# Performance work log

Hardware: AMD Instinct MI355X
Metric: run time of the kernel (lower is better)

## Reference

```python
import jax, jax.numpy as jnp
import numpy as np

MX_D, MN_D, CENTERS, WIDTH, SLOPE = 10.0, 0.0, 16, 1.0, 0.01
T_STEPS = 3


def _lrelu(x):
    return jax.nn.leaky_relu(x, SLOPE)


def _gauss(d):
    # d: [B,E,1] distances -> [B,E,CENTERS] gaussian radial basis
    mu = jnp.linspace(MN_D, MX_D, CENTERS, dtype=d.dtype)
    return jnp.exp(-jnp.square((d - mu[None, None, :]) / WIDTH))


def _equiv_message(v, idx2, n_recv, W1, W2, b, aw, ab):
    # v: [B,E,F] = concat(sender feats, receiver feats, bond feats).
    # Outer-product expand over receiver-cell axis (einsum with one-hot),
    # permutation-equivariant linear (local term + cell-sum term), LeakyReLU,
    # gather receiver cell, sigmoid attention gate, scatter_add to receivers.
    B, E, _ = v.shape
    O = W1.shape[1]
    oh = jax.nn.one_hot(idx2, n_recv, dtype=v.dtype)                 # [E,N]
    y_loc = jnp.einsum('bef,fo->beo', v, W1)                          # per-cell term
    y_sum = jnp.einsum('bef,fo->beo', v, W2) + b                      # cell-sum term (sum_n v*oh = v)
    y = _lrelu(y_loc[..., None] * oh[None, :, None, :] + y_sum[..., None])  # [B,E,O,N]
    gidx = jnp.broadcast_to(idx2[None, :, None, None], (B, E, O, 1))
    lat = jnp.take_along_axis(y, gidx, axis=3)[..., 0]                # [B,E,O]
    lat = jax.nn.sigmoid(lat @ aw + ab[None, None, :]) * lat          # attention gating
    return jnp.zeros((B, n_recv, O), v.dtype).at[:, idx2].add(lat)    # scatter_add over receivers


def _forward(sites, bonds, sites_p, bonds_sp, bonds_ps,
             se_W, se_b, sep_W, sep_b, ee_W, ee_b, eep_W, eep_b,
             eq_W1_ss, eq_W2_ss, eq_b_ss, att_w_ss, att_b_ss,
             eq_W1_ps, eq_W2_ps, eq_b_ps, att_w_ps, att_b_ps,
             eq_W1_sp, eq_W2_sp, eq_b_sp, att_w_sp, att_b_sp,
             nu_W1, nu_b1, nu_W2, nu_b2, nup_W1, nup_b1, nup_W2, nup_b2,
             p1_W, p1_b, p2a_W, p2a_b, p2b_W, p2b_b, p3_W, p3_b,
             idx1, idx2, idx1_sp, idx2_sp, idx1_ps, idx2_ps):
    s = _lrelu(sites @ se_W + se_b)          # [B,N,D] site embedding
    sp = _lrelu(sites_p @ sep_W + sep_b)     # [B,Np,D] pore embedding
    be = _lrelu(_gauss(bonds) @ ee_W + ee_b)
    bsp = _lrelu(_gauss(bonds_sp) @ eep_W + eep_b)
    bps = _lrelu(_gauss(bonds_ps) @ eep_W + eep_b)
    N, Np = s.shape[1], sp.shape[1]
    for t in range(T_STEPS):  # fixed number of message-passing layers
        v_ss = jnp.concatenate([s[:, idx1], s[:, idx2], be], -1)
        m = _equiv_message(v_ss, idx2, N, eq_W1_ss[t], eq_W2_ss[t], eq_b_ss[t], att_w_ss[t], att_b_ss[t])
        v_ps = jnp.concatenate([sp[:, idx1_ps], s[:, idx2_ps], bps], -1)
        m_ps = _equiv_message(v_ps, idx2_ps, N, eq_W1_ps[t], eq_W2_ps[t], eq_b_ps[t], att_w_ps[t], att_b_ps[t])
        v_sp = jnp.concatenate([s[:, idx1_sp], sp[:, idx2_sp], bsp], -1)
        m_sp = _equiv_message(v_sp, idx2_sp, Np, eq_W1_sp[t], eq_W2_sp[t], eq_b_sp[t], att_w_sp[t], att_b_sp[t])
        h = jnp.concatenate([s, m, m_ps], -1)
        h = _lrelu(_lrelu(h @ nu_W1[t] + nu_b1[t]) @ nu_W2[t] + nu_b2[t])
        s = s + h                              # residual node update (sites)
        hp = jnp.concatenate([sp, m_sp], -1)
        hp = _lrelu(_lrelu(hp @ nup_W1[t] + nup_b1[t]) @ nup_W2[t] + nup_b2[t])
        sp = sp + hp                           # residual node update (pores)
    x = _lrelu(s @ p1_W + p1_b).sum(1)        # sum pool over sites
    x = _lrelu(x @ p2a_W + p2a_b)
    x = _lrelu(x @ p2b_W + p2b_b)
    return x @ p3_W + p3_b                    # [B, out_size]


def setup_inputs():
    key = jax.random.key(0)
    ks = iter(jax.random.split(key, 80))
    B, N, Np, E, Esp = 4, 128, 16, 1280, 1024
    D, C, O, M, T = 32, CENTERS, 32, 64, T_STEPS
    Fin = 2 * D + 16  # sender + receiver + edge embedding

    def nrm(shape, fan):
        return jax.random.normal(next(ks), shape, jnp.float32) / np.float32(np.sqrt(fan))

    inp = {}
    inp['sites'] = jax.random.uniform(next(ks), (B, N, 1), jnp.float32)
    inp['bonds'] = jax.random.uniform(next(ks), (B, E, 1), jnp.float32) * MX_D
    inp['sites_p'] = jax.random.uniform(next(ks), (B, Np, 2), jnp.float32)
    inp['bonds_sp'] = jax.random.uniform(next(ks), (B, Esp, 1), jnp.float32) * MX_D
    inp['bonds_ps'] = jax.random.uniform(next(ks), (B, Esp, 1), jnp.float32) * MX_D
    inp['idx1'] = jax.random.randint(next(ks), (E,), 0, N, jnp.int32)
    inp['idx2'] = jax.random.randint(next(ks), (E,), 0, N, jnp.int32)
    inp['idx1_sp'] = jax.random.randint(next(ks), (Esp,), 0, N, jnp.int32)
    inp['idx2_sp'] = jax.random.randint(next(ks), (Esp,), 0, Np, jnp.int32)
    inp['idx1_ps'] = jax.random.randint(next(ks), (Esp,), 0, Np, jnp.int32)
    inp['idx2_ps'] = jax.random.randint(next(ks), (Esp,), 0, N, jnp.int32)
    # embeddings
    inp['se_W'] = nrm((1, D), 1); inp['se_b'] = nrm((D,), D)
    inp['sep_W'] = nrm((2, D), 2); inp['sep_b'] = nrm((D,), D)
    inp['ee_W'] = nrm((C, 16), C); inp['ee_b'] = nrm((16,), 16)
    inp['eep_W'] = nrm((C, 16), C); inp['eep_b'] = nrm((16,), 16)
    # equivariant message layers (stacked over T steps)
    for suf in ('ss', 'ps', 'sp'):
        inp['eq_W1_' + suf] = nrm((T, Fin, O), Fin)
        inp['eq_W2_' + suf] = nrm((T, Fin, O), Fin)
        inp['eq_b_' + suf] = nrm((T, O), O)
        inp['att_w_' + suf] = nrm((T, O, 1), O)
        inp['att_b_' + suf] = nrm((T, 1), 1)
    # node updates: sites take 2 message streams, pores take 1
    inp['nu_W1'] = nrm((T, D + 2 * O, D), D + 2 * O); inp['nu_b1'] = nrm((T, D), D)
    inp['nu_W2'] = nrm((T, D, D), D); inp['nu_b2'] = nrm((T, D), D)
    inp['nup_W1'] = nrm((T, D + O, D), D + O); inp['nup_b1'] = nrm((T, D), D)
    inp['nup_W2'] = nrm((T, D, D), D); inp['nup_b2'] = nrm((T, D), D)
    # prediction head
    inp['p1_W'] = nrm((D, M), D); inp['p1_b'] = nrm((M,), M)
    inp['p2a_W'] = nrm((M, M), M); inp['p2a_b'] = nrm((M,), M)
    inp['p2b_W'] = nrm((M, M), M); inp['p2b_b'] = nrm((M,), M)
    inp['p3_W'] = nrm((M, 1), M); inp['p3_b'] = nrm((1,), 1)
    return inp


def reference(sites, bonds, sites_p, bonds_sp, bonds_ps,
              se_W, se_b, sep_W, sep_b, ee_W, ee_b, eep_W, eep_b,
              eq_W1_ss, eq_W2_ss, eq_b_ss, att_w_ss, att_b_ss,
              eq_W1_ps, eq_W2_ps, eq_b_ps, att_w_ps, att_b_ps,
              eq_W1_sp, eq_W2_sp, eq_b_sp, att_w_sp, att_b_sp,
              nu_W1, nu_b1, nu_W2, nu_b2, nup_W1, nup_b1, nup_W2, nup_b2,
              p1_W, p1_b, p2a_W, p2a_b, p2b_W, p2b_b, p3_W, p3_b,
              idx1, idx2, idx1_sp, idx2_sp, idx1_ps, idx2_ps):
    return _forward(sites, bonds, sites_p, bonds_sp, bonds_ps,
                    se_W, se_b, sep_W, sep_b, ee_W, ee_b, eep_W, eep_b,
                    eq_W1_ss, eq_W2_ss, eq_b_ss, att_w_ss, att_b_ss,
                    eq_W1_ps, eq_W2_ps, eq_b_ps, att_w_ps, att_b_ps,
                    eq_W1_sp, eq_W2_sp, eq_b_sp, att_w_sp, att_b_sp,
                    nu_W1, nu_b1, nu_W2, nu_b2, nup_W1, nup_b1, nup_W2, nup_b2,
                    p1_W, p1_b, p2a_W, p2a_b, p2b_W, p2b_b, p3_W, p3_b,
                    idx1, idx2, idx1_sp, idx2_sp, idx1_ps, idx2_ps)
```

## Files before the change

kernel.cpp:

```cpp
#include <hip/hip_runtime.h>
#include <math.h>

#define BB   4
#define NN   128
#define NPP  16
#define EEE  1280
#define ESP  1024
#define DD   32
#define CC   16
#define OO   32
#define FIN  80
#define MMM  64
#define TT   3
#define TPB  256

#define MAXDEG_SS 48
#define MAXDEG_SP 192

constexpr int OFF_S    = 0;
constexpr int OFF_SP   = OFF_S   + BB*NN*DD;
constexpr int OFF_BE   = OFF_SP  + BB*NPP*DD;
constexpr int OFF_BSP  = OFF_BE  + BB*EEE*CC;
constexpr int OFF_BPS  = OFF_BSP + BB*ESP*CC;
constexpr int OFF_PRJ  = OFF_BPS + BB*ESP*CC;
constexpr int P_SASS = 0;
constexpr int P_SBSS = P_SASS + BB*NN*OO;
constexpr int P_SBPS = P_SBSS + BB*NN*OO;
constexpr int P_SASP = P_SBPS + BB*NN*OO;
constexpr int P_PAPS = P_SASP + BB*NN*OO;
constexpr int P_PBSP = P_PAPS + BB*NPP*OO;
constexpr int PRJ_SZ = P_PBSP + BB*NPP*OO;
constexpr int OFF_POOL = OFF_PRJ + 2*PRJ_SZ;
constexpr int OFF_CSR  = OFF_POOL + BB*MMM;
constexpr int SS_CNT  = 0;
constexpr int SS_LIST = SS_CNT + NN;
constexpr int PS_CNT  = SS_LIST + NN*MAXDEG_SS;
constexpr int PS_LIST = PS_CNT + NN;
constexpr int SP_CNT  = PS_LIST + NN*MAXDEG_SS;
constexpr int SP_LIST = SP_CNT + NPP;
constexpr int CSR_INTS = SP_LIST + NPP*MAXDEG_SP;
constexpr int TICKET   = CSR_INTS;

__device__ __forceinline__ float lrelu(float x) { return x > 0.f ? x : 0.01f * x; }

__device__ __forceinline__ float dot16(const float* ef, const float* sWe, int o) {
    float4 f0 = *(const float4*)(ef);
    float4 f1 = *(const float4*)(ef + 4);
    float4 f2 = *(const float4*)(ef + 8);
    float4 f3 = *(const float4*)(ef + 12);
    return f0.x*sWe[ 0*32+o] + f0.y*sWe[ 1*32+o] + f0.z*sWe[ 2*32+o] + f0.w*sWe[ 3*32+o]
         + f1.x*sWe[ 4*32+o] + f1.y*sWe[ 5*32+o] + f1.z*sWe[ 6*32+o] + f1.w*sWe[ 7*32+o]
         + f2.x*sWe[ 8*32+o] + f2.y*sWe[ 9*32+o] + f2.z*sWe[10*32+o] + f2.w*sWe[11*32+o]
         + f3.x*sWe[12*32+o] + f3.y*sWe[13*32+o] + f3.z*sWe[14*32+o] + f3.w*sWe[15*32+o];
}

__device__ __forceinline__ float red32(float r) {
#pragma unroll
    for (int mm = 16; mm > 0; mm >>= 1) r += __shfl_xor(r, mm, 32);
    return r;
}

__device__ __forceinline__ void edge_embed(float d, const float* W, const float* bvec, float* out) {
    float g[CC];
#pragma unroll
    for (int c = 0; c < CC; ++c) {
        float mu = (10.0f / 15.0f) * (float)c;
        float z = d - mu;
        g[c] = expf(-z * z);
    }
#pragma unroll
    for (int j = 0; j < CC; ++j) {
        float a = bvec[j];
#pragma unroll
        for (int c = 0; c < CC; ++c) a += g[c] * W[c * CC + j];
        out[j] = lrelu(a);
    }
}

__device__ __forceinline__ void csr_wave(const int* recv, int E, int r,
                                         int* cnt, int* list, int maxdeg, int lane) {
    int base = 0;
    for (int c = 0; c < E; c += 64) {
        const int e = c + lane;
        const bool m = (recv[e] == r);
        const unsigned long long mask = __ballot(m);
        if (m) {
            const int pos = base + __popcll(mask & ((1ull << lane) - 1ull));
            if (pos < maxdeg) list[pos] = e;
        }
        base += (int)__popcll(mask);
    }
    if (lane == 0) cnt[r] = base < maxdeg ? base : maxdeg;
}

__global__ __launch_bounds__(TPB) void k_init(
    const float* sites, const float* bonds, const float* sites_p,
    const float* bonds_sp, const float* bonds_ps,
    const int* idx2, const int* idx2_ps, const int* idx2_sp,
    const float* se_W, const float* se_b, const float* sep_W, const float* sep_b,
    const float* ee_W, const float* ee_b, const float* eep_W, const float* eep_b,
    const float* eqW1_ss, const float* eqW2_ss,
    const float* eqW1_ps, const float* eqW2_ps,
    const float* eqW1_sp, const float* eqW2_sp,
    float* ws)
{
    __shared__ float smem[4416];
    const int blk = blockIdx.x;
    const int tid = threadIdx.x;
    int* csr = (int*)(ws + OFF_CSR);

    if (blk == 0 && tid == 0) csr[TICKET] = 0;

    if (blk < 253) {
        const int totalA = BB*MMM + BB*EEE + BB*ESP + BB*ESP;
        for (int i = blk*TPB + tid; i < totalA; i += 253*TPB) {
            int r = i;
            if (r < BB*MMM) { ws[OFF_POOL + r] = 0.f; continue; }
            r -= BB*MMM;
            if (r < BB*EEE) { edge_embed(bonds[r],    ee_W,  ee_b,  ws + OFF_BE  + r*CC); continue; }
            r -= BB*EEE;
            if (r < BB*ESP) { edge_embed(bonds_sp[r], eep_W, eep_b, ws + OFF_BSP + r*CC); continue; }
            r -= BB*ESP;
            edge_embed(bonds_ps[r], eep_W, eep_b, ws + OFF_BPS + r*CC);
        }
    }
    if (blk < 72) {
        float* prj0 = ws + OFF_PRJ;
        const int el = tid >> 5, o = tid & 31;
        float* sP   = smem;
        float* sRow = smem + 4160;
        if (blk < 64) {
            const int g = blk*8 + el;
            float x = sites[g];
            float v0 = lrelu(x * se_W[o] + se_b[o]);
            ws[OFF_S + g*DD + o] = v0;
            sRow[el*32 + o] = v0;
            for (int i2 = tid; i2 < 4096; i2 += TPB) {
                int m = i2 >> 10, j = i2 & 1023, d = j >> 5, oo = j & 31;
                int row = (m == 1 || m == 2) ? (DD + d) : d;
                float wv;
                if (m < 2)      wv = eqW1_ss[row*OO + oo] + eqW2_ss[row*OO + oo];
                else if (m==2)  wv = eqW1_ps[row*OO + oo] + eqW2_ps[row*OO + oo];
                else            wv = eqW1_sp[row*OO + oo] + eqW2_sp[row*OO + oo];
                sP[i2] = wv;
            }
            __syncthreads();
            float p0=0.f,p1=0.f,p2=0.f,p3=0.f;
#pragma unroll
            for (int d = 0; d < 32; ++d) {
                float sv = sRow[el*32 + d];
                p0 += sv * sP[        d*32 + o];
                p1 += sv * sP[1024 +  d*32 + o];
                p2 += sv * sP[2048 +  d*32 + o];
                p3 += sv * sP[3072 +  d*32 + o];
            }
            prj0[P_SASS + g*OO + o] = p0;
            prj0[P_SBSS + g*OO + o] = p1;
            prj0[P_SBPS + g*OO + o] = p2;
            prj0[P_SASP + g*OO + o] = p3;
        } else {
            const int g = (blk-64)*8 + el;
            float x0 = sites_p[g*2], x1 = sites_p[g*2+1];
            float v0 = lrelu(x0 * sep_W[o] + x1 * sep_W[DD + o] + sep_b[o]);
            ws[OFF_SP + g*DD + o] = v0;
            sRow[el*32 + o] = v0;
            for (int i2 = tid; i2 < 2048; i2 += TPB) {
                int m = i2 >> 10, j = i2 & 1023, d = j >> 5, oo = j & 31;
                int row = (m == 0) ? d : (DD + d);
                float wv;
                if (m == 0) wv = eqW1_ps[row*OO + oo] + eqW2_ps[row*OO + oo];
                else        wv = eqW1_sp[row*OO + oo] + eqW2_sp[row*OO + oo];
                sP[i2] = wv;
            }
            __syncthreads();
            float p0=0.f,p1=0.f;
#pragma unroll
            for (int d = 0; d < 32; ++d) {
                float sv = sRow[el*32 + d];
                p0 += sv * sP[        d*32 + o];
                p1 += sv * sP[1024 +  d*32 + o];
            }
            prj0[P_PAPS + g*OO + o] = p0;
            prj0[P_PBSP + g*OO + o] = p1;
        }
    }
    if (blk >= 72 && blk < 140) {
        const int widx = (blk - 72) * 4 + (tid >> 6);
        const int lane = tid & 63;
        if (widx < NN) {
            csr_wave(idx2, EEE, widx, csr + SS_CNT, csr + SS_LIST + widx*MAXDEG_SS, MAXDEG_SS, lane);
        } else if (widx < 2*NN) {
            const int r = widx - NN;
            csr_wave(idx2_ps, ESP, r, csr + PS_CNT, csr + PS_LIST + r*MAXDEG_SS, MAXDEG_SS, lane);
        } else if (widx < 2*NN + NPP) {
            const int r = widx - 2*NN;
            csr_wave(idx2_sp, ESP, r, csr + SP_CNT, csr + SP_LIST + r*MAXDEG_SP, MAXDEG_SP, lane);
        }
    }
}

__global__ __launch_bounds__(TPB) void k_step(
    const float* eqW1_ss, const float* eqW2_ss, const float* eqb_ss, const float* aw_ss, const float* ab_ss,
    const float* eqW1_ps, const float* eqW2_ps, const float* eqb_ps, const float* aw_ps, const float* ab_ps,
    const float* eqW1_sp, const float* eqW2_sp, const float* eqb_sp, const float* aw_sp, const float* ab_sp,
    const int* idx1, const int* idx1_ps, const int* idx1_sp,
    const float* nuW1, const float* nub1, const float* nuW2, const float* nub2,
    const float* nupW1, const float* nupb1, const float* nupW2, const float* nupb2,
    const float* p1W, const float* p1b,
    const float* p2aW, const float* p2ab, const float* p2bW, const float* p2bb,
    const float* p3W, const float* p3b,
    float* ws, float* out, int t)
{
    __shared__ float sWe1[512], sWe2[512], sRed[512], sH[192], sU[64], sSnew[64];
    __shared__ int sWin;
    const int tid = threadIdx.x, blk = blockIdx.x;
    const int slot = tid >> 5, o = tid & 31;
    const int par = t & 1;
    const float* PRJ  = ws + OFF_PRJ + par * PRJ_SZ;
    float*       PRJn = ws + OFF_PRJ + (par ^ 1) * PRJ_SZ;
    const int* csr = (const int*)(ws + OFF_CSR);

    if (blk < 256) {
        const int r = slot >> 2, q = slot & 3;
        for (int i = tid; i < 512; i += TPB) {
            sWe1[i] = eqW1_ss[t*FIN*OO + 2*DD*OO + i] + eqW2_ss[t*FIN*OO + 2*DD*OO + i];
            sWe2[i] = eqW1_ps[t*FIN*OO + 2*DD*OO + i] + eqW2_ps[t*FIN*OO + 2*DD*OO + i];
        }
        __syncthreads();
        const int g = blk*2 + r, b = g >> 7, n = g & 127;
        const float bias_ss = eqb_ss[t*OO+o], awo_ss = aw_ss[t*OO+o], abs_ss = ab_ss[t];
        const float bias_ps = eqb_ps[t*OO+o], awo_ps = aw_ps[t*OO+o], abs_ps = ab_ps[t];
        const float sb_ss = PRJ[P_SBSS + g*OO + o];
        const float sb_ps = PRJ[P_SBPS + g*OO + o];
        const float* SAss = PRJ + P_SASS + b*(NN*OO);
        const float* PAps = PRJ + P_PAPS + b*(NPP*OO);
        const float* BEb  = ws + OFF_BE  + b*(EEE*CC);
        const float* BPSb = ws + OFF_BPS + b*(ESP*CC);
        float acc_ss = 0.f, acc_ps = 0.f;
        {
            const int cnt = csr[SS_CNT + n];
            const int* lst = csr + SS_LIST + n*MAXDEG_SS;
            for (int k = q; k < cnt; k += 4) {
                const int e = lst[k];
                const int s1 = idx1[e];
                float a = bias_ss + sb_ss + SAss[s1*OO + o] + dot16(BEb + e*CC, sWe1, o);
                float u = lrelu(a);
                float rr = red32(u * awo_ss);
                acc_ss += u / (1.f + expf(-(rr + abs_ss)));
            }
        }
        {
            const int cnt = csr[PS_CNT + n];
            const int* lst = csr + PS_LIST + n*MAXDEG_SS;
            for (int k = q; k < cnt; k += 4) {
                const int e = lst[k];
                const int s1 = idx1_ps[e];
                float a = bias_ps + sb_ps + PAps[s1*OO + o] + dot16(BPSb + e*CC, sWe2, o);
                float u = lrelu(a);
                float rr = red32(u * awo_ps);
                acc_ps += u / (1.f + expf(-(rr + abs_ps)));
            }
        }
        sRed[slot*64 + o]      = acc_ss;
        sRed[slot*64 + 32 + o] = acc_ps;
        if (tid < 64) sH[(tid>>5)*96 + (tid&31)] = ws[OFF_S + (blk*2 + (tid>>5))*DD + (tid&31)];
        __syncthreads();
        if (tid < 128) {
            const int r2 = tid >> 6, c = tid & 63;
            sH[r2*96 + 32 + c] = sRed[(r2*4  )*64 + c] + sRed[(r2*4+1)*64 + c]
                               + sRed[(r2*4+2)*64 + c] + sRed[(r2*4+3)*64 + c];
        }
        __syncthreads();
        if (tid < 64) {
            const int r2 = tid >> 5, oo = tid & 31;
            const float* W1 = nuW1 + t*(96*32);
            float a = nub1[t*32 + oo];
#pragma unroll
            for (int f = 0; f < 96; ++f) a += sH[r2*96 + f] * W1[f*32 + oo];
            sU[r2*32 + oo] = lrelu(a);
        }
        __syncthreads();
        if (tid < 64) {
            const int r2 = tid >> 5, oo = tid & 31;
            const float* W2 = nuW2 + t*(32*32);
            float a = nub2[t*32 + oo];
#pragma unroll
            for (int k2 = 0; k2 < 32; ++k2) a += sU[r2*32 + k2] * W2[k2*32 + oo];
            const float snew = sH[r2*96 + oo] + lrelu(a);
            ws[OFF_S + (blk*2 + r2)*DD + oo] = snew;
            sSnew[r2*32 + oo] = snew;
        }
        __syncthreads();
        if (t < TT-1) {
            const int tn = t + 1;
            const int r2 = slot >> 2, m = slot & 3;
            const int g2 = blk*2 + r2;
            const float *w1m, *w2m; float* dst;
            if (m == 0)      { w1m = eqW1_ss + tn*FIN*OO;         w2m = eqW2_ss + tn*FIN*OO;         dst = PRJn + P_SASS; }
            else if (m == 1) { w1m = eqW1_ss + tn*FIN*OO + DD*OO; w2m = eqW2_ss + tn*FIN*OO + DD*OO; dst = PRJn + P_SBSS; }
            else if (m == 2) { w1m = eqW1_ps + tn*FIN*OO + DD*OO; w2m = eqW2_ps + tn*FIN*OO + DD*OO; dst = PRJn + P_SBPS; }
            else             { w1m = eqW1_sp + tn*FIN*OO;         w2m = eqW2_sp + tn*FIN*OO;         dst = PRJn + P_SASP; }
            float a = 0.f;
#pragma unroll
            for (int d = 0; d < 32; ++d) a += sSnew[r2*32 + d] * (w1m[d*OO + o] + w2m[d*OO + o]);
            dst[g2*OO + o] = a;
        } else {
            if (tid < 128) {
                const int r2 = tid >> 6, mm = tid & 63;
                const int g2 = blk*2 + r2, b2 = g2 >> 7;
                float a = p1b[mm];
#pragma unroll
                for (int d = 0; d < 32; ++d) a += sSnew[r2*32 + d] * p1W[d*MMM + mm];
                atomicAdd(&ws[OFF_POOL + b2*MMM + mm], lrelu(a));
            }
            __syncthreads();
            if (tid == 0) {
                int* ticket = (int*)(ws + OFF_CSR) + TICKET;
                int p = __hip_atomic_fetch_add(ticket, 1, __ATOMIC_ACQ_REL, __HIP_MEMORY_SCOPE_AGENT);
                sWin = (p == 255) ? 1 : 0;
            }
            __syncthreads();
            if (sWin) {
                float* sx = sWe1;
                float* sy = sWe2;
                float* sz = sRed;
                sx[tid] = __hip_atomic_load(&ws[OFF_POOL + tid], __ATOMIC_RELAXED, __HIP_MEMORY_SCOPE_AGENT);
                __syncthreads();
                const int b2 = tid >> 6, mm = tid & 63;
                float a = p2ab[mm];
#pragma unroll
                for (int k = 0; k < MMM; ++k) a += sx[b2*64 + k] * p2aW[k*MMM + mm];
                sy[tid] = lrelu(a);
                __syncthreads();
                a = p2bb[mm];
#pragma unroll
                for (int k = 0; k < MMM; ++k) a += sy[b2*64 + k] * p2bW[k*MMM + mm];
                sz[tid] = lrelu(a);
                __syncthreads();
                if (tid < BB) {
                    float acc = p3b[0];
#pragma unroll
                    for (int k = 0; k < MMM; ++k) acc += sz[tid*64 + k] * p3W[k];
                    out[tid] = acc;
                }
            }
        }
    } else {
        for (int i = tid; i < 512; i += TPB)
            sWe1[i] = eqW1_sp[t*FIN*OO + 2*DD*OO + i] + eqW2_sp[t*FIN*OO + 2*DD*OO + i];
        __syncthreads();
        const int g = blk - 256, b = g >> 4, p = g & 15;
        const float bias_sp = eqb_sp[t*OO+o], awo_sp = aw_sp[t*OO+o], abs_sp = ab_sp[t];
        const float sb_sp = PRJ[P_PBSP + g*OO + o];
        const float* SAsp = PRJ + P_SASP + b*(NN*OO);
        const float* BSPb = ws + OFF_BSP + b*(ESP*CC);
        float acc_sp = 0.f;
        {
            const int cnt = csr[SP_CNT + p];
            const int* lst = csr + SP_LIST + p*MAXDEG_SP;
            for (int k = slot; k < cnt; k += 8) {
                const int e = lst[k];
                const int s1 = idx1_sp[e];
                float a = bias_sp + sb_sp + SAsp[s1*OO + o] + dot16(BSPb + e*CC, sWe1, o);
                float u = lrelu(a);
                float rr = red32(u * awo_sp);
                acc_sp += u / (1.f + expf(-(rr + abs_sp)));
            }
        }
        sRed[slot*32 + o] = acc_sp;
        if (tid < 32) sH[tid] = ws[OFF_SP + g*DD + tid];
        __syncthreads();
        if (tid < 32) {
            float mv = 0.f;
#pragma unroll
            for (int s2 = 0; s2 < 8; ++s2) mv += sRed[s2*32 + tid];
            sH[32 + tid] = mv;
        }
        __syncthreads();
        if (tid < 32) {
            const float* W1 = nupW1 + t*(64*32);
            float a = nupb1[t*32 + tid];
#pragma unroll
            for (int f = 0; f < 64; ++f) a += sH[f] * W1[f*32 + tid];
            sU[tid] = lrelu(a);
        }
        __syncthreads();
        if (tid < 32) {
            const float* W2 = nupW2 + t*(32*32);
            float a = nupb2[t*32 + tid];
#pragma unroll
            for (int k2 = 0; k2 < 32; ++k2) a += sU[k2] * W2[k2*32 + tid];
            const float snew = sH[tid] + lrelu(a);
            ws[OFF_SP + g*DD + tid] = snew;
            sSnew[tid] = snew;
        }
        __syncthreads();
        if (t < TT-1 && tid < 64) {
            const int tn = t + 1;
            const int m = tid >> 5, oo = tid & 31;
            const float *w1m, *w2m; float* dst;
            if (m == 0) { w1m = eqW1_ps + tn*FIN*OO;         w2m = eqW2_ps + tn*FIN*OO;         dst = PRJn + P_PAPS; }
            else        { w1m = eqW1_sp + tn*FIN*OO + DD*OO; w2m = eqW2_sp + tn*FIN*OO + DD*OO; dst = PRJn + P_PBSP; }
            float a = 0.f;
#pragma unroll
            for (int d = 0; d < 32; ++d) a += sSnew[d] * (w1m[d*OO + oo] + w2m[d*OO + oo]);
            dst[g*OO + oo] = a;
        }
    }
}

extern "C" void kernel_launch(void* const* d_in, const int* in_sizes, int n_in,
                              void* d_out, int out_size, void* d_ws, size_t ws_size,
                              hipStream_t stream) {
    (void)in_sizes; (void)n_in; (void)out_size; (void)ws_size;
    const float* sites    = (const float*)d_in[0];
    const float* bonds    = (const float*)d_in[1];
    const float* sites_p  = (const float*)d_in[2];
    const float* bonds_sp = (const float*)d_in[3];
    const float* bonds_ps = (const float*)d_in[4];
    const int* idx1    = (const int*)d_in[5];
    const int* idx2    = (const int*)d_in[6];
    const int* idx1_sp = (const int*)d_in[7];
    const int* idx2_sp = (const int*)d_in[8];
    const int* idx1_ps = (const int*)d_in[9];
    const int* idx2_ps = (const int*)d_in[10];
    const float* se_W  = (const float*)d_in[11];
    const float* se_b  = (const float*)d_in[12];
    const float* sep_W = (const float*)d_in[13];
    const float* sep_b = (const float*)d_in[14];
    const float* ee_W  = (const float*)d_in[15];
    const float* ee_b  = (const float*)d_in[16];
    const float* eep_W = (const float*)d_in[17];
    const float* eep_b = (const float*)d_in[18];
    const float* eqW1_ss = (const float*)d_in[19];
    const float* eqW2_ss = (const float*)d_in[20];
    const float* eqb_ss  = (const float*)d_in[21];
    const float* aw_ss   = (const float*)d_in[22];
    const float* ab_ss   = (const float*)d_in[23];
    const float* eqW1_ps = (const float*)d_in[24];
    const float* eqW2_ps = (const float*)d_in[25];
    const float* eqb_ps  = (const float*)d_in[26];
    const float* aw_ps   = (const float*)d_in[27];
    const float* ab_ps   = (const float*)d_in[28];
    const float* eqW1_sp = (const float*)d_in[29];
    const float* eqW2_sp = (const float*)d_in[30];
    const float* eqb_sp  = (const float*)d_in[31];
    const float* aw_sp   = (const float*)d_in[32];
    const float* ab_sp   = (const float*)d_in[33];
    const float* nuW1  = (const float*)d_in[34];
    const float* nub1  = (const float*)d_in[35];
    const float* nuW2  = (const float*)d_in[36];
    const float* nub2  = (const float*)d_in[37];
    const float* nupW1 = (const float*)d_in[38];
    const float* nupb1 = (const float*)d_in[39];
    const float* nupW2 = (const float*)d_in[40];
    const float* nupb2 = (const float*)d_in[41];
    const float* p1W  = (const float*)d_in[42];
    const float* p1b  = (const float*)d_in[43];
    const float* p2aW = (const float*)d_in[44];
    const float* p2ab = (const float*)d_in[45];
    const float* p2bW = (const float*)d_in[46];
    const float* p2bb = (const float*)d_in[47];
    const float* p3W  = (const float*)d_in[48];
    const float* p3b  = (const float*)d_in[49];

    float* ws  = (float*)d_ws;
    float* out = (float*)d_out;

    k_init<<<256, TPB, 0, stream>>>(sites, bonds, sites_p, bonds_sp, bonds_ps,
                                    idx2, idx2_ps, idx2_sp,
                                    se_W, se_b, sep_W, sep_b, ee_W, ee_b, eep_W, eep_b,
                                    eqW1_ss, eqW2_ss, eqW1_ps, eqW2_ps, eqW1_sp, eqW2_sp, ws);
    for (int t = 0; t < TT; ++t) {
        k_step<<<320, TPB, 0, stream>>>(
            eqW1_ss, eqW2_ss, eqb_ss, aw_ss, ab_ss,
            eqW1_ps, eqW2_ps, eqb_ps, aw_ps, ab_ps,
            eqW1_sp, eqW2_sp, eqb_sp, aw_sp, ab_sp,
            idx1, idx1_ps, idx1_sp,
            nuW1, nub1, nuW2, nub2, nupW1, nupb1, nupW2, nupb2,
            p1W, p1b, p2aW, p2ab, p2bW, p2bb, p3W, p3b,
            ws, out, t);
    }
}
```

Baseline: 55.53 us.

## Fuse init kernel into first message-passing step, recomputing embeddings on the fly

Replaces the separate init kernel and the t=0 step kernel with a single fused step-0 kernel. Each block builds its receiver CSR lists locally, recomputes site, pore and edge embeddings per edge instead of reading precomputed projections, and writes edge features and next-step projections for later steps. Pool and ticket reset move into the t=1 step. This removes one launch and a global round trip, at the cost of redundant embedding and CSR scans done in every block.

```diff
diff --git a/kernel.cpp b/kernel.cpp
--- a/kernel.cpp
+++ b/kernel.cpp
@@ -60,141 +60,316 @@
     return r;
 }
 
-__device__ __forceinline__ void edge_embed(float d, const float* W, const float* bvec, float* out) {
-    float g[CC];
-#pragma unroll
-    for (int c = 0; c < CC; ++c) {
-        float mu = (10.0f / 15.0f) * (float)c;
-        float z = d - mu;
-        g[c] = expf(-z * z);
-    }
-#pragma unroll
-    for (int j = 0; j < CC; ++j) {
-        float a = bvec[j];
-#pragma unroll
-        for (int c = 0; c < CC; ++c) a += g[c] * W[c * CC + j];
-        out[j] = lrelu(a);
-    }
-}
-
-__device__ __forceinline__ void csr_wave(const int* recv, int E, int r,
-                                         int* cnt, int* list, int maxdeg, int lane) {
-    int base = 0;
-    for (int c = 0; c < E; c += 64) {
-        const int e = c + lane;
-        const bool m = (recv[e] == r);
-        const unsigned long long mask = __ballot(m);
-        if (m) {
-            const int pos = base + __popcll(mask & ((1ull << lane) - 1ull));
-            if (pos < maxdeg) list[pos] = e;
-        }
-        base += (int)__popcll(mask);
-    }
-    if (lane == 0) cnt[r] = base < maxdeg ? base : maxdeg;
-}
-
-__global__ __launch_bounds__(TPB) void k_init(
+__global__ __launch_bounds__(TPB) void k_step0(
     const float* sites, const float* bonds, const float* sites_p,
     const float* bonds_sp, const float* bonds_ps,
-    const int* idx2, const int* idx2_ps, const int* idx2_sp,
+    const int* idx1, const int* idx2, const int* idx1_ps, const int* idx2_ps,
+    const int* idx1_sp, const int* idx2_sp,
     const float* se_W, const float* se_b, const float* sep_W, const float* sep_b,
     const float* ee_W, const float* ee_b, const float* eep_W, const float* eep_b,
-    const float* eqW1_ss, const float* eqW2_ss,
-    const float* eqW1_ps, const float* eqW2_ps,
-    const float* eqW1_sp, const float* eqW2_sp,
+    const float* eqW1_ss, const float* eqW2_ss, const float* eqb_ss, const float* aw_ss, const float* ab_ss,
+    const float* eqW1_ps, const float* eqW2_ps, const float* eqb_ps, const float* aw_ps, const float* ab_ps,
+    const float* eqW1_sp, const float* eqW2_sp, const float* eqb_sp, const float* aw_sp, const float* ab_sp,
+    const float* nuW1, const float* nub1, const float* nuW2, const float* nub2,
+    const float* nupW1, const float* nupb1, const float* nupW2, const float* nupb2,
     float* ws)
 {
-    __shared__ float smem[4416];
-    const int blk = blockIdx.x;
-    const int tid = threadIdx.x;
+    __shared__ float sWA1[1024], sWA2[1024], sWB1[1024], sWB2[1024];
+    __shared__ float sWE1[512], sWE2[512];
+    __shared__ float sEWa[272], sEWb[272];
+    __shared__ float sEmb[160];
+    __shared__ int2  sLany[192];
+    __shared__ int   sCnt[4];
+    __shared__ float sRed[512], sH[192], sU[64], sSnew[64];
+
+    const int tid = threadIdx.x, blk = blockIdx.x;
+    const int slot = tid >> 5, o = tid & 31;
     int* csr = (int*)(ws + OFF_CSR);
-
-    if (blk == 0 && tid == 0) csr[TICKET] = 0;
-
-    if (blk < 253) {
-        const int totalA = BB*MMM + BB*EEE + BB*ESP + BB*ESP;
-        for (int i = blk*TPB + tid; i < totalA; i += 253*TPB) {
-            int r = i;
-            if (r < BB*MMM) { ws[OFF_POOL + r] = 0.f; continue; }
-            r -= BB*MMM;
-            if (r < BB*EEE) { edge_embed(bonds[r],    ee_W,  ee_b,  ws + OFF_BE  + r*CC); continue; }
-            r -= BB*EEE;
-            if (r < BB*ESP) { edge_embed(bonds_sp[r], eep_W, eep_b, ws + OFF_BSP + r*CC); continue; }
-            r -= BB*ESP;
-            edge_embed(bonds_ps[r], eep_W, eep_b, ws + OFF_BPS + r*CC);
-        }
-    }
-    if (blk < 72) {
-        float* prj0 = ws + OFF_PRJ;
-        const int el = tid >> 5, o = tid & 31;
-        float* sP   = smem;
-        float* sRow = smem + 4160;
-        if (blk < 64) {
-            const int g = blk*8 + el;
-            float x = sites[g];
-            float v0 = lrelu(x * se_W[o] + se_b[o]);
-            ws[OFF_S + g*DD + o] = v0;
-            sRow[el*32 + o] = v0;
-            for (int i2 = tid; i2 < 4096; i2 += TPB) {
-                int m = i2 >> 10, j = i2 & 1023, d = j >> 5, oo = j & 31;
-                int row = (m == 1 || m == 2) ? (DD + d) : d;
-                float wv;
-                if (m < 2)      wv = eqW1_ss[row*OO + oo] + eqW2_ss[row*OO + oo];
-                else if (m==2)  wv = eqW1_ps[row*OO + oo] + eqW2_ps[row*OO + oo];
-                else            wv = eqW1_sp[row*OO + oo] + eqW2_sp[row*OO + oo];
-                sP[i2] = wv;
-            }
-            __syncthreads();
-            float p0=0.f,p1=0.f,p2=0.f,p3=0.f;
+    float* PRJn = ws + OFF_PRJ + 1 * PRJ_SZ;
+
+    if (blk < 256) {
+        const int b  = (blk*2) >> 7;
+        const int n0 = (blk*2) & 127;
+        {
+            const int w = tid >> 6, lane = tid & 63;
+            const int nw = n0 + (w & 1);
+            const int* recvp = (w < 2) ? idx2 : idx2_ps;
+            const int* sendp = (w < 2) ? idx1 : idx1_ps;
+            const int Ew     = (w < 2) ? EEE : ESP;
+            int2* ldst = sLany + w*48;
+            int*  gcnt = csr + ((w < 2) ? SS_CNT : PS_CNT);
+            int*  glst = csr + ((w < 2) ? (SS_LIST + nw*MAXDEG_SS) : (PS_LIST + nw*MAXDEG_SS));
+            int base = 0;
+            for (int c = 0; c < Ew; c += 64) {
+                const int e = c + lane;
+                const bool m = (recvp[e] == nw);
+                const unsigned long long mask = __ballot(m);
+                if (m) {
+                    const int pos = base + __popcll(mask & ((1ull << lane) - 1ull));
+                    if (pos < MAXDEG_SS) {
+                        ldst[pos] = make_int2(e, sendp[e]);
+                        if (b == 0) glst[pos] = e;
+                    }
+                }
+                base += (int)__popcll(mask);
+            }
+            if (lane == 0) {
+                int cc = base < MAXDEG_SS ? base : MAXDEG_SS;
+                sCnt[w] = cc;
+                if (b == 0) gcnt[nw] = cc;
+            }
+        }
+        for (int i = tid; i < 1024; i += TPB) {
+            sWA1[i] = eqW1_ss[i]        + eqW2_ss[i];
+            sWB1[i] = eqW1_ss[1024 + i] + eqW2_ss[1024 + i];
+            sWA2[i] = eqW1_ps[i]        + eqW2_ps[i];
+            sWB2[i] = eqW1_ps[1024 + i] + eqW2_ps[1024 + i];
+        }
+        for (int i = tid; i < 512; i += TPB) {
+            sWE1[i] = eqW1_ss[2048 + i] + eqW2_ss[2048 + i];
+            sWE2[i] = eqW1_ps[2048 + i] + eqW2_ps[2048 + i];
+        }
+        if (tid < 256) { sEWa[tid] = ee_W[tid]; sEWb[tid] = eep_W[tid]; }
+        if (tid < 16)  { sEWa[256+tid] = ee_b[tid]; sEWb[256+tid] = eep_b[tid]; }
+        if (tid < 32) {
+            sEmb[tid]      = se_W[tid];
+            sEmb[32+tid]   = se_b[tid];
+            sEmb[64+tid]   = sep_W[tid];
+            sEmb[96+tid]   = sep_W[32+tid];
+            sEmb[128+tid]  = sep_b[tid];
+        }
+        __syncthreads();
+
+        const int r = slot >> 2, q = slot & 3;
+        const int g = blk*2 + r;
+        float acc_ss = 0.f, acc_ps = 0.f;
+        {
+            const float x_r = sites[g];
+            float sb_ss = 0.f, sb_ps = 0.f;
 #pragma unroll
             for (int d = 0; d < 32; ++d) {
-                float sv = sRow[el*32 + d];
-                p0 += sv * sP[        d*32 + o];
-                p1 += sv * sP[1024 +  d*32 + o];
-                p2 += sv * sP[2048 +  d*32 + o];
-                p3 += sv * sP[3072 +  d*32 + o];
-            }
-            prj0[P_SASS + g*OO + o] = p0;
-            prj0[P_SBSS + g*OO + o] = p1;
-            prj0[P_SBPS + g*OO + o] = p2;
-            prj0[P_SASP + g*OO + o] = p3;
-        } else {
-            const int g = (blk-64)*8 + el;
-            float x0 = sites_p[g*2], x1 = sites_p[g*2+1];
-            float v0 = lrelu(x0 * sep_W[o] + x1 * sep_W[DD + o] + sep_b[o]);
-            ws[OFF_SP + g*DD + o] = v0;
-            sRow[el*32 + o] = v0;
-            for (int i2 = tid; i2 < 2048; i2 += TPB) {
-                int m = i2 >> 10, j = i2 & 1023, d = j >> 5, oo = j & 31;
-                int row = (m == 0) ? d : (DD + d);
-                float wv;
-                if (m == 0) wv = eqW1_ps[row*OO + oo] + eqW2_ps[row*OO + oo];
-                else        wv = eqW1_sp[row*OO + oo] + eqW2_sp[row*OO + oo];
-                sP[i2] = wv;
-            }
-            __syncthreads();
-            float p0=0.f,p1=0.f;
-#pragma unroll
-            for (int d = 0; d < 32; ++d) {
-                float sv = sRow[el*32 + d];
-                p0 += sv * sP[        d*32 + o];
-                p1 += sv * sP[1024 +  d*32 + o];
-            }
-            prj0[P_PAPS + g*OO + o] = p0;
-            prj0[P_PBSP + g*OO + o] = p1;
-        }
-    }
-    if (blk >= 72 && blk < 140) {
-        const int widx = (blk - 72) * 4 + (tid >> 6);
-        const int lane = tid & 63;
-        if (widx < NN) {
-            csr_wave(idx2, EEE, widx, csr + SS_CNT, csr + SS_LIST + widx*MAXDEG_SS, MAXDEG_SS, lane);
-        } else if (widx < 2*NN) {
-            const int r = widx - NN;
-            csr_wave(idx2_ps, ESP, r, csr + PS_CNT, csr + PS_LIST + r*MAXDEG_SS, MAXDEG_SS, lane);
-        } else if (widx < 2*NN + NPP) {
-            const int r = widx - 2*NN;
-            csr_wave(idx2_sp, ESP, r, csr + SP_CNT, csr + SP_LIST + r*MAXDEG_SP, MAXDEG_SP, lane);
+                float s0d = lrelu(x_r*sEmb[d] + sEmb[32+d]);
+                sb_ss += s0d * sWB1[d*32 + o];
+                sb_ps += s0d * sWB2[d*32 + o];
+            }
+            {
+                const float bias = eqb_ss[o], awo = aw_ss[o], abv = ab_ss[0];
+                const int cnt = sCnt[r];
+                const int2* lst = sLany + r*48;
+                for (int k = q; k < cnt; k += 4) {
+                    const int2 es = lst[k];
+                    const float xs = sites[b*NN + es.y];
+                    float SA = 0.f;
+#pragma unroll
+                    for (int d = 0; d < 32; ++d)
+                        SA += lrelu(xs*sEmb[d] + sEmb[32+d]) * sWA1[d*32 + o];
+                    const float bv = bonds[b*EEE + es.x];
+                    float gg[16];
+#pragma unroll
+                    for (int c = 0; c < 16; ++c) { float z = bv - (10.f/15.f)*c; gg[c] = expf(-z*z); }
+                    float edot = 0.f, myef = 0.f;
+#pragma unroll
+                    for (int j = 0; j < 16; ++j) {
+                        float ej = sEWa[256+j];
+#pragma unroll
+                        for (int c = 0; c < 16; ++c) ej += gg[c]*sEWa[c*16+j];
+                        ej = lrelu(ej);
+                        edot += ej * sWE1[j*32 + o];
+                        if (o == j) myef = ej;
+                    }
+                    if (o < 16) ws[OFF_BE + (b*EEE + es.x)*CC + o] = myef;
+                    float u = lrelu(bias + sb_ss + SA + edot);
+                    float rr = red32(u * awo);
+                    acc_ss += u / (1.f + expf(-(rr + abv)));
+                }
+            }
+            {
+                const float bias = eqb_ps[o], awo = aw_ps[o], abv = ab_ps[0];
+                const int cnt = sCnt[2 + r];
+                const int2* lst = sLany + (2 + r)*48;
+                for (int k = q; k < cnt; k += 4) {
+                    const int2 es = lst[k];
+                    const float xp0 = sites_p[(b*NPP + es.y)*2];
+                    const float xp1 = sites_p[(b*NPP + es.y)*2 + 1];
+                    float SA = 0.f;
+#pragma unroll
+                    for (int d = 0; d < 32; ++d)
+                        SA += lrelu(xp0*sEmb[64+d] + xp1*sEmb[96+d] + sEmb[128+d]) * sWA2[d*32 + o];
+                    const float bv = bonds_ps[b*ESP + es.x];
+                    float gg[16];
+#pragma unroll
+                    for (int c = 0; c < 16; ++c) { float z = bv - (10.f/15.f)*c; gg[c] = expf(-z*z); }
+                    float edot = 0.f, myef = 0.f;
+#pragma unroll
+                    for (int j = 0; j < 16; ++j) {
+                        float ej = sEWb[256+j];
+#pragma unroll
+                        for (int c = 0; c < 16; ++c) ej += gg[c]*sEWb[c*16+j];
+                        ej = lrelu(ej);
+                        edot += ej * sWE2[j*32 + o];
+                        if (o == j) myef = ej;
+                    }
+                    if (o < 16) ws[OFF_BPS + (b*ESP + es.x)*CC + o] = myef;
+                    float u = lrelu(bias + sb_ps + SA + edot);
+                    float rr = red32(u * awo);
+                    acc_ps += u / (1.f + expf(-(rr + abv)));
+                }
+            }
+        }
+        sRed[slot*64 + o]      = acc_ss;
+        sRed[slot*64 + 32 + o] = acc_ps;
+        if (tid < 64) {
+            const int e2 = tid >> 5, oo = tid & 31;
+            sH[e2*96 + oo] = lrelu(sites[blk*2 + e2]*sEmb[oo] + sEmb[32+oo]);
+        }
+        __syncthreads();
+        if (tid < 128) {
+            const int r2 = tid >> 6, c = tid & 63;
+            sH[r2*96 + 32 + c] = sRed[(r2*4  )*64 + c] + sRed[(r2*4+1)*64 + c]
+                               + sRed[(r2*4+2)*64 + c] + sRed[(r2*4+3)*64 + c];
+        }
+        __syncthreads();
+        if (tid < 64) {
+            const int r2 = tid >> 5, oo = tid & 31;
+            float a = nub1[oo];
+#pragma unroll
+            for (int f = 0; f < 96; ++f) a += sH[r2*96 + f] * nuW1[f*32 + oo];
+            sU[r2*32 + oo] = lrelu(a);
+        }
+        __syncthreads();
+        if (tid < 64) {
+            const int r2 = tid >> 5, oo = tid & 31;
+            float a = nub2[oo];
+#pragma unroll
+            for (int k2 = 0; k2 < 32; ++k2) a += sU[r2*32 + k2] * nuW2[k2*32 + oo];
+            const float snew = sH[r2*96 + oo] + lrelu(a);
+            ws[OFF_S + (blk*2 + r2)*DD + oo] = snew;
+            sSnew[r2*32 + oo] = snew;
+        }
+        __syncthreads();
+        {
+            const int r2 = slot >> 2, m = slot & 3;
+            const int g2 = blk*2 + r2;
+            const float *w1m, *w2m; float* dst;
+            if (m == 0)      { w1m = eqW1_ss + 1*FIN*OO;         w2m = eqW2_ss + 1*FIN*OO;         dst = PRJn + P_SASS; }
+            else if (m == 1) { w1m = eqW1_ss + 1*FIN*OO + DD*OO; w2m = eqW2_ss + 1*FIN*OO + DD*OO; dst = PRJn + P_SBSS; }
+            else if (m == 2) { w1m = eqW1_ps + 1*FIN*OO + DD*OO; w2m = eqW2_ps + 1*FIN*OO + DD*OO; dst = PRJn + P_SBPS; }
+            else             { w1m = eqW1_sp + 1*FIN*OO;         w2m = eqW2_sp + 1*FIN*OO;         dst = PRJn + P_SASP; }
+            float a = 0.f;
+#pragma unroll
+            for (int d = 0; d < 32; ++d) a += sSnew[r2*32 + d] * (w1m[d*OO + o] + w2m[d*OO + o]);
+            dst[g2*OO + o] = a;
+        }
+    } else {
+        const int pg = blk - 256, b = pg >> 4, p = pg & 15;
+        if (tid < 64) {
+            const int lane = tid;
+            int base = 0;
+            for (int c = 0; c < ESP; c += 64) {
+                const int e = c + lane;
+                const bool m = (idx2_sp[e] == p);
+                const unsigned long long mask = __ballot(m);
+                if (m) {
+                    const int pos = base + __popcll(mask & ((1ull << lane) - 1ull));
+                    if (pos < MAXDEG_SP) {
+                        sLany[pos] = make_int2(e, idx1_sp[e]);
+                        if (b == 0) csr[SP_LIST + p*MAXDEG_SP + pos] = e;
+                    }
+                }
+                base += (int)__popcll(mask);
+            }
+            if (lane == 0) {
+                int cc = base < MAXDEG_SP ? base : MAXDEG_SP;
+                sCnt[0] = cc;
+                if (b == 0) csr[SP_CNT + p] = cc;
+            }
+        }
+        for (int i = tid; i < 1024; i += TPB) {
+            sWA1[i] = eqW1_sp[i]        + eqW2_sp[i];
+            sWB1[i] = eqW1_sp[1024 + i] + eqW2_sp[1024 + i];
+        }
+        for (int i = tid; i < 512; i += TPB)
+            sWE1[i] = eqW1_sp[2048 + i] + eqW2_sp[2048 + i];
+        if (tid < 256) sEWa[tid] = eep_W[tid];
+        if (tid < 16)  sEWa[256+tid] = eep_b[tid];
+        if (tid < 32) {
+            sEmb[tid]      = se_W[tid];
+            sEmb[32+tid]   = se_b[tid];
+            sEmb[64+tid]   = sep_W[tid];
+            sEmb[96+tid]   = sep_W[32+tid];
+            sEmb[128+tid]  = sep_b[tid];
+        }
+        __syncthreads();
+
+        const float xp0 = sites_p[pg*2], xp1 = sites_p[pg*2 + 1];
+        float sb = 0.f;
+#pragma unroll
+        for (int d = 0; d < 32; ++d)
+            sb += lrelu(xp0*sEmb[64+d] + xp1*sEmb[96+d] + sEmb[128+d]) * sWB1[d*32 + o];
+        const float bias = eqb_sp[o], awo = aw_sp[o], abv = ab_sp[0];
+        const int cnt = sCnt[0];
+        float acc = 0.f;
+        for (int k = slot; k < cnt; k += 8) {
+            const int2 es = sLany[k];
+            const float xs = sites[b*NN + es.y];
+            float SA = 0.f;
+#pragma unroll
+            for (int d = 0; d < 32; ++d)
+                SA += lrelu(xs*sEmb[d] + sEmb[32+d]) * sWA1[d*32 + o];
+            const float bv = bonds_sp[b*ESP + es.x];
+            float gg[16];
+#pragma unroll
+            for (int c = 0; c < 16; ++c) { float z = bv - (10.f/15.f)*c; gg[c] = expf(-z*z); }
+            float edot = 0.f, myef = 0.f;
+#pragma unroll
+            for (int j = 0; j < 16; ++j) {
+                float ej = sEWa[256+j];
+#pragma unroll
+                for (int c = 0; c < 16; ++c) ej += gg[c]*sEWa[c*16+j];
+                ej = lrelu(ej);
+                edot += ej * sWE1[j*32 + o];
+                if (o == j) myef = ej;
+            }
+            if (o < 16) ws[OFF_BSP + (b*ESP + es.x)*CC + o] = myef;
+            float u = lrelu(bias + sb + SA + edot);
+            float rr = red32(u * awo);
+            acc += u / (1.f + expf(-(rr + abv)));
+        }
+        sRed[slot*32 + o] = acc;
+        if (tid < 32) sH[tid] = lrelu(xp0*sEmb[64+tid] + xp1*sEmb[96+tid] + sEmb[128+tid]);
+        __syncthreads();
+        if (tid < 32) {
+            float mv = 0.f;
+#pragma unroll
+            for (int s2 = 0; s2 < 8; ++s2) mv += sRed[s2*32 + tid];
+            sH[32 + tid] = mv;
+        }
+        __syncthreads();
+        if (tid < 32) {
+            float a = nupb1[tid];
+#pragma unroll
+            for (int f = 0; f < 64; ++f) a += sH[f] * nupW1[f*32 + tid];
+            sU[tid] = lrelu(a);
+        }
+        __syncthreads();
+        if (tid < 32) {
+            float a = nupb2[tid];
+#pragma unroll
+            for (int k2 = 0; k2 < 32; ++k2) a += sU[k2] * nupW2[k2*32 + tid];
+            const float snew = sH[tid] + lrelu(a);
+            ws[OFF_SP + pg*DD + tid] = snew;
+            sSnew[tid] = snew;
+        }
+        __syncthreads();
+        if (tid < 64) {
+            const int m = slot, oo = tid & 31;
+            const float *w1m, *w2m; float* dst;
+            if (m == 0) { w1m = eqW1_ps + 1*FIN*OO;         w2m = eqW2_ps + 1*FIN*OO;         dst = PRJn + P_PAPS; }
+            else        { w1m = eqW1_sp + 1*FIN*OO + DD*OO; w2m = eqW2_sp + 1*FIN*OO + DD*OO; dst = PRJn + P_PBSP; }
+            float a = 0.f;
+#pragma unroll
+            for (int d = 0; d < 32; ++d) a += sSnew[d] * (w1m[d*OO + oo] + w2m[d*OO + oo]);
+            dst[pg*OO + oo] = a;
         }
     }
 }
@@ -220,6 +395,11 @@
     float*       PRJn = ws + OFF_PRJ + (par ^ 1) * PRJ_SZ;
     const int* csr = (const int*)(ws + OFF_CSR);
 
+    if (t == 1 && blk == 0) {
+        ws[OFF_POOL + tid] = 0.f;
+        if (tid == 0) ((int*)(ws + OFF_CSR))[TICKET] = 0;
+    }
+
     if (blk < 256) {
         const int r = slot >> 2, q = slot & 3;
         for (int i = tid; i < 512; i += TPB) {
@@ -292,9 +472,9 @@
         }
         __syncthreads();
         if (t < TT-1) {
-            const int tn = t + 1;
             const int r2 = slot >> 2, m = slot & 3;
             const int g2 = blk*2 + r2;
+            const int tn = t + 1;
             const float *w1m, *w2m; float* dst;
             if (m == 0)      { w1m = eqW1_ss + tn*FIN*OO;         w2m = eqW2_ss + tn*FIN*OO;         dst = PRJn + P_SASS; }
             else if (m == 1) { w1m = eqW1_ss + tn*FIN*OO + DD*OO; w2m = eqW2_ss + tn*FIN*OO + DD*OO; dst = PRJn + P_SBSS; }
@@ -467,11 +647,15 @@
     float* ws  = (float*)d_ws;
     float* out = (float*)d_out;
 
-    k_init<<<256, TPB, 0, stream>>>(sites, bonds, sites_p, bonds_sp, bonds_ps,
-                                    idx2, idx2_ps, idx2_sp,
-                                    se_W, se_b, sep_W, sep_b, ee_W, ee_b, eep_W, eep_b,
-                                    eqW1_ss, eqW2_ss, eqW1_ps, eqW2_ps, eqW1_sp, eqW2_sp, ws);
-    for (int t = 0; t < TT; ++t) {
+    k_step0<<<320, TPB, 0, stream>>>(
+        sites, bonds, sites_p, bonds_sp, bonds_ps,
+        idx1, idx2, idx1_ps, idx2_ps, idx1_sp, idx2_sp,
+        se_W, se_b, sep_W, sep_b, ee_W, ee_b, eep_W, eep_b,
+        eqW1_ss, eqW2_ss, eqb_ss, aw_ss, ab_ss,
+        eqW1_ps, eqW2_ps, eqb_ps, aw_ps, ab_ps,
+        eqW1_sp, eqW2_sp, eqb_sp, aw_sp, ab_sp,
+        nuW1, nub1, nuW2, nub2, nupW1, nupb1, nupW2, nupb2, ws);
+    for (int t = 1; t < TT; ++t) {
         k_step<<<320, TPB, 0, stream>>>(
             eqW1_ss, eqW2_ss, eqb_ss, aw_ss, ab_ss,
             eqW1_ps, eqW2_ps, eqb_ps, aw_ps, ab_ps,
```

Result: slower. 106.7 us (+92.1%).
